# Kernel tuning notes

Hardware: AMD Instinct MI355X
Metric: run time of the kernel (lower is better)

## Reference

```python
import jax, jax.numpy as jnp
import numpy as np

N_NODES = 25000
N_EDGES = 400000
CHANNELS = 32
EDGE_FEAT_DIM = 8
HIDDEN = 64
NUM_IRREPS = 4  # messages irreps = 2x0e + 2x1o -> 4 irreps, dim 8
AVG_NUM_NEIGHBORS = 16.0


def _mlp(x, W0, W1, W2, W3):
    # e3nn MultiLayerPerceptron: dense layers with 1/sqrt(fan_in) forward
    # normalization, silu on hidden layers, no output activation.
    for W in (W0, W1, W2):
        x = jax.nn.silu(x @ (W / jnp.sqrt(jnp.float32(W.shape[0]))))
    return x @ (W3 / jnp.sqrt(jnp.float32(W3.shape[0])))


def setup_inputs() -> dict:
    key = jax.random.key(0)
    ks = jax.random.split(key, 9)
    node_feats = jax.random.normal(ks[0], (N_NODES, CHANNELS, 4), jnp.float32)
    edge_attrs = jax.random.normal(ks[1], (N_EDGES, 4), jnp.float32)
    edge_feats = jax.random.normal(ks[2], (N_EDGES, EDGE_FEAT_DIM), jnp.float32)
    senders = jax.random.randint(ks[3], (N_EDGES,), 0, N_NODES)
    receivers = jax.random.randint(ks[4], (N_EDGES,), 0, N_NODES)
    W0 = jax.random.normal(ks[5], (EDGE_FEAT_DIM, HIDDEN), jnp.float32)
    W1 = jax.random.normal(ks[6], (HIDDEN, HIDDEN), jnp.float32)
    W2 = jax.random.normal(ks[7], (HIDDEN, HIDDEN), jnp.float32)
    W3 = jax.random.normal(ks[8], (HIDDEN, CHANNELS * NUM_IRREPS), jnp.float32)
    return {"node_feats": node_feats, "edge_attrs": edge_attrs,
            "edge_feats": edge_feats, "senders": senders, "receivers": receivers,
            "W0": W0, "W1": W1, "W2": W2, "W3": W3}


def reference(node_feats, edge_attrs, edge_feats, senders, receivers, W0, W1, W2, W3):
    # Gather sender node features: [E, C, 4] with irreps 0e (dim1) + 1o (dim3)
    x = node_feats[senders]
    s, v = x[..., 0], x[..., 1:4]            # [E,C], [E,C,3]
    a_s = edge_attrs[:, 0]                   # Y_0: [E]
    a_v = edge_attrs[:, 1:4]                 # Y_1: [E,3]

    # CG tensor product filtered to 0e + 1o (e3nn normalization: sqrt(2l3+1)*w3j)
    m0a = s * a_s[:, None]                                   # 0e x 0e -> 0e  [E,C]
    m0b = jnp.einsum('ecd,ed->ec', v, a_v) / jnp.sqrt(3.0)   # 1o x 1o -> 0e  [E,C]
    m1a = s[..., None] * a_v[:, None, :]                     # 0e x 1o -> 1o  [E,C,3]
    m1b = v * a_s[:, None, None]                             # 1o x 0e -> 1o  [E,C,3]

    # Edge MLP gate: [E, C*num_irreps] -> mul_to_axis -> [E, C, num_irreps]
    mix = _mlp(edge_feats, W0, W1, W2, W3).reshape(N_EDGES, CHANNELS, NUM_IRREPS)

    # Elementwise tensor product with 4x0e scalars: per-irrep gating
    out_s = jnp.stack([m0a * mix[..., 0], m0b * mix[..., 1]], axis=-1)          # [E,C,2]
    out_v = jnp.concatenate([m1a * mix[..., 2:3], m1b * mix[..., 3:4]], axis=-1)  # [E,C,6]
    messages = jnp.concatenate([out_s, out_v], axis=-1)                          # [E,C,8]

    # Scatter-add into receivers, then normalize by sqrt(avg_num_neighbors)
    agg = jax.ops.segment_sum(messages, receivers, num_segments=N_NODES)
    return agg / jnp.sqrt(AVG_NUM_NEIGHBORS)
```

## Files before the change

kernel.cpp:

```cpp
#include <hip/hip_runtime.h>
#include <hip/hip_fp16.h>

#define NE 400000
#define NN 25000
#define MAXDEG 56
#define LDS_STRIDE 65

typedef __attribute__((ext_vector_type(8))) _Float16 half8;
typedef __attribute__((ext_vector_type(4))) _Float16 half4;
typedef __attribute__((ext_vector_type(4))) float f32x4;

#define WS_MIX_OFF   0ull
#define WS_SLOTS_OFF 102400000ull
#define WS_CNT_OFF   108000000ull
#define WS_WBUF_OFF  108100000ull
#define WS_NEED      108136864ull

#define WB_L0 0
#define WB_L1 2048
#define WB_L2 6144
#define WB_L3 10240

__device__ __forceinline__ float fast_silu(float x) {
    float e = __expf(-x);
    return x * __builtin_amdgcn_rcpf(1.0f + e);
}

__global__ __launch_bounds__(64) void prep_weights(
    const float* __restrict__ W0, const float* __restrict__ W1,
    const float* __restrict__ W2, const float* __restrict__ W3,
    _Float16* __restrict__ wbuf)
{
    const int f    = blockIdx.x;
    const int lane = threadIdx.x;
    const int n    = lane & 15;
    const int quad = lane >> 4;

    const float* W; int K, N, kt, nt, fl, base; float scale;
    if (f < 4)       { W = W0; K = 8;  N = 64;  fl = f;      kt = 0;       nt = fl;     scale = 0.35355339059327373f; base = WB_L0; }
    else if (f < 12) { W = W1; K = 64; N = 64;  fl = f - 4;  kt = fl >> 2; nt = fl & 3; scale = 0.125f;   base = WB_L1; }
    else if (f < 20) { W = W2; K = 64; N = 64;  fl = f - 12; kt = fl >> 2; nt = fl & 3; scale = 0.125f;   base = WB_L2; }
    else             { W = W3; K = 64; N = 128; fl = f - 20; kt = fl >> 3; nt = fl & 7; scale = 0.03125f; base = WB_L3; }

    _Float16 v[8];
    #pragma unroll
    for (int j = 0; j < 8; ++j) {
        const int k = kt * 32 + quad * 8 + j;
        const float val = (k < K) ? W[k * N + nt * 16 + n] * scale : 0.0f;
        v[j] = (_Float16)val;
    }
    *(half8*)(wbuf + base + fl * 512 + lane * 8) = *(const half8*)v;
}

__global__ __launch_bounds__(256) void build_kernel(
    const int* __restrict__ receivers, int* __restrict__ cnt, int* __restrict__ slots)
{
    int e = blockIdx.x * 256 + threadIdx.x;
    if (e >= NE) return;
    int r = receivers[e];
    int s = atomicAdd(&cnt[r], 1);
    if (s < MAXDEG) slots[r * MAXDEG + s] = e;
}

#define HS 72
__global__ __launch_bounds__(256) void mlp_mfma_kernel(
    const float*    __restrict__ edge_feats,
    const _Float16* __restrict__ wbuf,
    _Float16*       __restrict__ mix16)
{
    __shared__ _Float16 H[4 * 16 * HS];
    const int wave = threadIdx.x >> 6;
    const int lane = threadIdx.x & 63;
    const int col  = lane & 15;
    const int quad = lane >> 4;
    const int e0   = (blockIdx.x * 4 + wave) * 16;

    _Float16* Hw = &H[wave * 16 * HS];
    const half8* wb = (const half8*)wbuf;
    const f32x4 zero4 = {0.f, 0.f, 0.f, 0.f};

    half8 b0 = {0, 0, 0, 0, 0, 0, 0, 0};
    if (quad == 0) {
        const float4* efp = (const float4*)(edge_feats + (size_t)(e0 + col) * 8);
        const float4 x = efp[0], y = efp[1];
        b0[0] = (_Float16)x.x; b0[1] = (_Float16)x.y; b0[2] = (_Float16)x.z; b0[3] = (_Float16)x.w;
        b0[4] = (_Float16)y.x; b0[5] = (_Float16)y.y; b0[6] = (_Float16)y.z; b0[7] = (_Float16)y.w;
    }

    {
        #pragma unroll
        for (int nt = 0; nt < 4; ++nt) {
            f32x4 acc = __builtin_amdgcn_mfma_f32_16x16x32_f16(wb[(WB_L0 / 512 + nt) * 64 + lane], b0, zero4, 0, 0, 0);
            half4 h;
            #pragma unroll
            for (int r = 0; r < 4; ++r) h[r] = (_Float16)fast_silu(acc[r]);
            *(half4*)&Hw[col * HS + nt * 16 + quad * 4] = h;
        }
    }

    #pragma unroll
    for (int layer = 0; layer < 2; ++layer) {
        const int wbase = (layer == 0 ? WB_L1 : WB_L2) / 512;
        const half8 blo = *(const half8*)&Hw[col * HS + 0  + quad * 8];
        const half8 bhi = *(const half8*)&Hw[col * HS + 32 + quad * 8];
        f32x4 acc[4];
        #pragma unroll
        for (int nt = 0; nt < 4; ++nt) {
            acc[nt] = __builtin_amdgcn_mfma_f32_16x16x32_f16(wb[(wbase + 0 + nt) * 64 + lane], blo, zero4, 0, 0, 0);
            acc[nt] = __builtin_amdgcn_mfma_f32_16x16x32_f16(wb[(wbase + 4 + nt) * 64 + lane], bhi, acc[nt], 0, 0, 0);
        }
        #pragma unroll
        for (int nt = 0; nt < 4; ++nt) {
            half4 h;
            #pragma unroll
            for (int r = 0; r < 4; ++r) h[r] = (_Float16)fast_silu(acc[nt][r]);
            *(half4*)&Hw[col * HS + nt * 16 + quad * 4] = h;
        }
    }

    {
        const half8 blo = *(const half8*)&Hw[col * HS + 0  + quad * 8];
        const half8 bhi = *(const half8*)&Hw[col * HS + 32 + quad * 8];
        _Float16* mrow = mix16 + (size_t)(e0 + col) * 128;
        #pragma unroll
        for (int nt = 0; nt < 8; ++nt) {
            f32x4 acc = __builtin_amdgcn_mfma_f32_16x16x32_f16(wb[(WB_L3 / 512 + 0 + nt) * 64 + lane], blo, zero4, 0, 0, 0);
            acc = __builtin_amdgcn_mfma_f32_16x16x32_f16(wb[(WB_L3 / 512 + 8 + nt) * 64 + lane], bhi, acc, 0, 0, 0);
            half4 h;
            #pragma unroll
            for (int r = 0; r < 4; ++r) h[r] = (_Float16)acc[r];
            *(half4*)&mrow[nt * 16 + quad * 4] = h;
        }
    }
}

__global__ __launch_bounds__(64) void gather_kernel(
    const float*    __restrict__ node_feats,
    const float*    __restrict__ edge_attrs,
    const int*      __restrict__ senders,
    const _Float16* __restrict__ mix16,
    const int*      __restrict__ cnt,
    const int*      __restrict__ slots,
    float*          __restrict__ out)
{
    const int n    = blockIdx.x;
    const int lane = threadIdx.x;
    const int g    = lane >> 4;
    const int s    = lane & 15;
    const int c0   = 2 * s;
    const float inv_sqrt3 = 0.5773502691896258f;

    int d = cnt[n];
    if (d > MAXDEG) d = MAXDEG;
    const int* sl = slots + n * MAXDEG;

    float acc[16];
    #pragma unroll
    for (int j = 0; j < 16; ++j) acc[j] = 0.0f;

    #pragma unroll 2
    for (int base = 0; base < d; base += 4) {
        const int  ei  = base + g;
        const bool act = (ei < d);
        const int  eic = act ? ei : 0;
        const int  eid = sl[eic];
        const int  snd = senders[eid];
        const float4 a4v = ((const float4*)edge_attrs)[eid];
        const half8 m8 = *(const half8*)(mix16 + (size_t)eid * 128 + c0 * 4);
        const float4 xA = ((const float4*)(node_feats + (size_t)snd * 128))[c0];
        const float4 xB = ((const float4*)(node_feats + (size_t)snd * 128))[c0 + 1];

        const float z = act ? 1.0f : 0.0f;
        const float as = a4v.x, av0 = a4v.y, av1 = a4v.z, av2 = a4v.w;

        {
            const float m0 = z * (float)m8[0], m1 = z * (float)m8[1];
            const float m2 = z * (float)m8[2], m3 = z * (float)m8[3];
            const float sc = xA.x, v0 = xA.y, v1 = xA.z, v2 = xA.w;
            acc[0] = fmaf(sc * as, m0, acc[0]);
            const float dv = v0 * av0 + v1 * av1 + v2 * av2;
            acc[1] = fmaf(dv * inv_sqrt3, m1, acc[1]);
            acc[2] = fmaf(sc * av0, m2, acc[2]);
            acc[3] = fmaf(sc * av1, m2, acc[3]);
            acc[4] = fmaf(sc * av2, m2, acc[4]);
            acc[5] = fmaf(v0 * as, m3, acc[5]);
            acc[6] = fmaf(v1 * as, m3, acc[6]);
            acc[7] = fmaf(v2 * as, m3, acc[7]);
        }
        {
            const float m0 = z * (float)m8[4], m1 = z * (float)m8[5];
            const float m2 = z * (float)m8[6], m3 = z * (float)m8[7];
            const float sc = xB.x, v0 = xB.y, v1 = xB.z, v2 = xB.w;
            acc[8]  = fmaf(sc * as, m0, acc[8]);
            const float dv = v0 * av0 + v1 * av1 + v2 * av2;
            acc[9]  = fmaf(dv * inv_sqrt3, m1, acc[9]);
            acc[10] = fmaf(sc * av0, m2, acc[10]);
            acc[11] = fmaf(sc * av1, m2, acc[11]);
            acc[12] = fmaf(sc * av2, m2, acc[12]);
            acc[13] = fmaf(v0 * as, m3, acc[13]);
            acc[14] = fmaf(v1 * as, m3, acc[14]);
            acc[15] = fmaf(v2 * as, m3, acc[15]);
        }
    }

    #pragma unroll
    for (int j = 0; j < 16; ++j) {
        acc[j] += __shfl_xor(acc[j], 16, 64);
        acc[j] += __shfl_xor(acc[j], 32, 64);
    }

    if (g == 0) {
        float4* op = (float4*)(out + (size_t)n * 256 + s * 16);
        float4 r0; r0.x = acc[0];  r0.y = acc[1];  r0.z = acc[2];  r0.w = acc[3];
        float4 r1; r1.x = acc[4];  r1.y = acc[5];  r1.z = acc[6];  r1.w = acc[7];
        float4 r2; r2.x = acc[8];  r2.y = acc[9];  r2.z = acc[10]; r2.w = acc[11];
        float4 r3; r3.x = acc[12]; r3.y = acc[13]; r3.z = acc[14]; r3.w = acc[15];
        op[0] = r0; op[1] = r1; op[2] = r2; op[3] = r3;
    }
}

__global__ __launch_bounds__(128) void edge_mp_kernel(
    const float* __restrict__ node_feats, const float* __restrict__ edge_attrs,
    const float* __restrict__ edge_feats, const int* __restrict__ senders,
    const int* __restrict__ receivers, const float* __restrict__ W0,
    const float* __restrict__ W1, const float* __restrict__ W2,
    const float* __restrict__ W3, float* __restrict__ out)
{
    __shared__ float hbuf[128 * LDS_STRIDE];
    const int tid = threadIdx.x;
    const int e   = blockIdx.x * 128 + tid;
    if (e >= NE) return;
    float* hl = &hbuf[tid * LDS_STRIDE];

    float4 ef0 = ((const float4*)edge_feats)[e * 2 + 0];
    float4 ef1 = ((const float4*)edge_feats)[e * 2 + 1];
    float ef[8] = {ef0.x, ef0.y, ef0.z, ef0.w, ef1.x, ef1.y, ef1.z, ef1.w};
    float acc[64];
    #pragma unroll
    for (int i = 0; i < 64; ++i) acc[i] = 0.0f;
    #pragma unroll
    for (int j = 0; j < 8; ++j) {
        const float xj = ef[j];
        const float* wrow = W0 + j * 64;
        #pragma unroll
        for (int i = 0; i < 64; ++i) acc[i] = fmaf(xj, wrow[i], acc[i]);
    }
    {
        const float s0 = 0.35355339059327373f;
        #pragma unroll
        for (int i = 0; i < 64; ++i) hl[i] = fast_silu(acc[i] * s0);
    }
    #pragma unroll
    for (int i = 0; i < 64; ++i) acc[i] = 0.0f;
    #pragma unroll 4
    for (int j = 0; j < 64; ++j) {
        const float xj = hl[j];
        const float* wrow = W1 + j * 64;
        #pragma unroll
        for (int i = 0; i < 64; ++i) acc[i] = fmaf(xj, wrow[i], acc[i]);
    }
    #pragma unroll
    for (int i = 0; i < 64; ++i) hl[i] = fast_silu(acc[i] * 0.125f);
    #pragma unroll
    for (int i = 0; i < 64; ++i) acc[i] = 0.0f;
    #pragma unroll 4
    for (int j = 0; j < 64; ++j) {
        const float xj = hl[j];
        const float* wrow = W2 + j * 64;
        #pragma unroll
        for (int i = 0; i < 64; ++i) acc[i] = fmaf(xj, wrow[i], acc[i]);
    }
    float h2[64];
    #pragma unroll
    for (int i = 0; i < 64; ++i) h2[i] = fast_silu(acc[i] * 0.125f);

    const int snd = senders[e];
    const int rcv = receivers[e];
    const float4 a4 = ((const float4*)edge_attrs)[e];
    const float a_s = a4.x, av0 = a4.y, av1 = a4.z, av2 = a4.w;
    const float4* nf4 = (const float4*)(node_feats + (size_t)snd * 128);
    float* outp = out + (size_t)rcv * 256;
    const float mixscale = 0.03125f;
    const float inv_sqrt3 = 0.5773502691896258f;

    #pragma unroll 2
    for (int c = 0; c < 32; ++c) {
        float m0 = 0.0f, m1 = 0.0f, m2 = 0.0f, m3 = 0.0f;
        const float* wc = W3 + c * 4;
        #pragma unroll
        for (int j = 0; j < 64; ++j) {
            const float hj = h2[j];
            m0 = fmaf(hj, wc[j * 128 + 0], m0);
            m1 = fmaf(hj, wc[j * 128 + 1], m1);
            m2 = fmaf(hj, wc[j * 128 + 2], m2);
            m3 = fmaf(hj, wc[j * 128 + 3], m3);
        }
        m0 *= mixscale; m1 *= mixscale; m2 *= mixscale; m3 *= mixscale;
        const float4 x4 = nf4[c];
        const float s = x4.x, v0 = x4.y, v1 = x4.z, v2 = x4.w;
        float* op = outp + c * 8;
        atomicAdd(op + 0, s * a_s * m0);
        const float dotva = v0 * av0 + v1 * av1 + v2 * av2;
        atomicAdd(op + 1, dotva * inv_sqrt3 * m1);
        atomicAdd(op + 2, s * av0 * m2);
        atomicAdd(op + 3, s * av1 * m2);
        atomicAdd(op + 4, s * av2 * m2);
        atomicAdd(op + 5, v0 * a_s * m3);
        atomicAdd(op + 6, v1 * a_s * m3);
        atomicAdd(op + 7, v2 * a_s * m3);
    }
}

extern "C" void kernel_launch(void* const* d_in, const int* in_sizes, int n_in,
                              void* d_out, int out_size, void* d_ws, size_t ws_size,
                              hipStream_t stream) {
    const float* node_feats = (const float*)d_in[0];
    const float* edge_attrs = (const float*)d_in[1];
    const float* edge_feats = (const float*)d_in[2];
    const int*   senders    = (const int*)d_in[3];
    const int*   receivers  = (const int*)d_in[4];
    const float* W0 = (const float*)d_in[5];
    const float* W1 = (const float*)d_in[6];
    const float* W2 = (const float*)d_in[7];
    const float* W3 = (const float*)d_in[8];
    float* outp = (float*)d_out;

    if (ws_size >= WS_NEED) {
        char* w = (char*)d_ws;
        _Float16* mix16 = (_Float16*)(w + WS_MIX_OFF);
        int*      slots = (int*)(w + WS_SLOTS_OFF);
        int*      cnt   = (int*)(w + WS_CNT_OFF);
        _Float16* wbuf  = (_Float16*)(w + WS_WBUF_OFF);

        hipMemsetAsync(cnt, 0, NN * sizeof(int), stream);
        hipLaunchKernelGGL(prep_weights, dim3(36), dim3(64), 0, stream,
                           W0, W1, W2, W3, wbuf);
        hipLaunchKernelGGL(build_kernel, dim3((NE + 255) / 256), dim3(256), 0, stream,
                           receivers, cnt, slots);
        hipLaunchKernelGGL(mlp_mfma_kernel, dim3(NE / 64), dim3(256), 0, stream,
                           edge_feats, wbuf, mix16);
        hipLaunchKernelGGL(gather_kernel, dim3(NN), dim3(64), 0, stream,
                           node_feats, edge_attrs, senders, mix16, cnt, slots, outp);
    } else {
        hipMemsetAsync(d_out, 0, (size_t)out_size * sizeof(float), stream);
        hipLaunchKernelGGL(edge_mp_kernel, dim3((NE + 127) / 128), dim3(128), 0, stream,
                           node_feats, edge_attrs, edge_feats, senders, receivers,
                           W0, W1, W2, W3, outp);
    }
}
```

Before: 229.4 us.

## Fuse edge MLP into per-node gather kernel, dropping the mix buffer

Merges the edge MLP kernel into the receiver-sorted gather kernel. Each wave now handles one node, evaluates the MLP on MFMA for that node's incoming edges in tiles of 16, and stages the gates in LDS rather than writing and rereading a 100 MB fp16 mix array in global memory. The cost is that MFMA tiles are partly empty when a node's degree is not a multiple of 16, which adds extra MLP compute, and the per-node work becomes more serialized.

```diff
diff --git a/kernel.cpp b/kernel.cpp
--- a/kernel.cpp
+++ b/kernel.cpp
@@ -10,11 +10,10 @@
 typedef __attribute__((ext_vector_type(4))) _Float16 half4;
 typedef __attribute__((ext_vector_type(4))) float f32x4;
 
-#define WS_MIX_OFF   0ull
-#define WS_SLOTS_OFF 102400000ull
-#define WS_CNT_OFF   108000000ull
-#define WS_WBUF_OFF  108100000ull
-#define WS_NEED      108136864ull
+#define WS_SLOTS_OFF 0ull
+#define WS_CNT_OFF   5600000ull
+#define WS_WBUF_OFF  5700000ull
+#define WS_NEED      5736864ull
 
 #define WB_L0 0
 #define WB_L1 2048
@@ -63,143 +62,135 @@
 }
 
 #define HS 72
-__global__ __launch_bounds__(256) void mlp_mfma_kernel(
+#define MS 136
+__global__ __launch_bounds__(256) void fused_node_kernel(
+    const float*    __restrict__ node_feats,
+    const float*    __restrict__ edge_attrs,
     const float*    __restrict__ edge_feats,
+    const int*      __restrict__ senders,
     const _Float16* __restrict__ wbuf,
-    _Float16*       __restrict__ mix16)
+    const int*      __restrict__ cnt,
+    const int*      __restrict__ slots,
+    float*          __restrict__ out)
 {
     __shared__ _Float16 H[4 * 16 * HS];
+    __shared__ _Float16 Mx[4 * 16 * MS];
     const int wave = threadIdx.x >> 6;
     const int lane = threadIdx.x & 63;
     const int col  = lane & 15;
     const int quad = lane >> 4;
-    const int e0   = (blockIdx.x * 4 + wave) * 16;
+    const int n    = blockIdx.x * 4 + wave;
+    const float inv_sqrt3 = 0.5773502691896258f;
 
     _Float16* Hw = &H[wave * 16 * HS];
+    _Float16* Mw = &Mx[wave * 16 * MS];
     const half8* wb = (const half8*)wbuf;
     const f32x4 zero4 = {0.f, 0.f, 0.f, 0.f};
-
-    half8 b0 = {0, 0, 0, 0, 0, 0, 0, 0};
-    if (quad == 0) {
-        const float4* efp = (const float4*)(edge_feats + (size_t)(e0 + col) * 8);
-        const float4 x = efp[0], y = efp[1];
-        b0[0] = (_Float16)x.x; b0[1] = (_Float16)x.y; b0[2] = (_Float16)x.z; b0[3] = (_Float16)x.w;
-        b0[4] = (_Float16)y.x; b0[5] = (_Float16)y.y; b0[6] = (_Float16)y.z; b0[7] = (_Float16)y.w;
-    }
-
-    {
-        #pragma unroll
-        for (int nt = 0; nt < 4; ++nt) {
-            f32x4 acc = __builtin_amdgcn_mfma_f32_16x16x32_f16(wb[(WB_L0 / 512 + nt) * 64 + lane], b0, zero4, 0, 0, 0);
-            half4 h;
-            #pragma unroll
-            for (int r = 0; r < 4; ++r) h[r] = (_Float16)fast_silu(acc[r]);
-            *(half4*)&Hw[col * HS + nt * 16 + quad * 4] = h;
-        }
-    }
-
-    #pragma unroll
-    for (int layer = 0; layer < 2; ++layer) {
-        const int wbase = (layer == 0 ? WB_L1 : WB_L2) / 512;
-        const half8 blo = *(const half8*)&Hw[col * HS + 0  + quad * 8];
-        const half8 bhi = *(const half8*)&Hw[col * HS + 32 + quad * 8];
-        f32x4 acc[4];
-        #pragma unroll
-        for (int nt = 0; nt < 4; ++nt) {
-            acc[nt] = __builtin_amdgcn_mfma_f32_16x16x32_f16(wb[(wbase + 0 + nt) * 64 + lane], blo, zero4, 0, 0, 0);
-            acc[nt] = __builtin_amdgcn_mfma_f32_16x16x32_f16(wb[(wbase + 4 + nt) * 64 + lane], bhi, acc[nt], 0, 0, 0);
-        }
-        #pragma unroll
-        for (int nt = 0; nt < 4; ++nt) {
-            half4 h;
-            #pragma unroll
-            for (int r = 0; r < 4; ++r) h[r] = (_Float16)fast_silu(acc[nt][r]);
-            *(half4*)&Hw[col * HS + nt * 16 + quad * 4] = h;
-        }
-    }
-
-    {
-        const half8 blo = *(const half8*)&Hw[col * HS + 0  + quad * 8];
-        const half8 bhi = *(const half8*)&Hw[col * HS + 32 + quad * 8];
-        _Float16* mrow = mix16 + (size_t)(e0 + col) * 128;
-        #pragma unroll
-        for (int nt = 0; nt < 8; ++nt) {
-            f32x4 acc = __builtin_amdgcn_mfma_f32_16x16x32_f16(wb[(WB_L3 / 512 + 0 + nt) * 64 + lane], blo, zero4, 0, 0, 0);
-            acc = __builtin_amdgcn_mfma_f32_16x16x32_f16(wb[(WB_L3 / 512 + 8 + nt) * 64 + lane], bhi, acc, 0, 0, 0);
-            half4 h;
-            #pragma unroll
-            for (int r = 0; r < 4; ++r) h[r] = (_Float16)acc[r];
-            *(half4*)&mrow[nt * 16 + quad * 4] = h;
-        }
-    }
-}
-
-__global__ __launch_bounds__(64) void gather_kernel(
-    const float*    __restrict__ node_feats,
-    const float*    __restrict__ edge_attrs,
-    const int*      __restrict__ senders,
-    const _Float16* __restrict__ mix16,
-    const int*      __restrict__ cnt,
-    const int*      __restrict__ slots,
-    float*          __restrict__ out)
-{
-    const int n    = blockIdx.x;
-    const int lane = threadIdx.x;
-    const int g    = lane >> 4;
-    const int s    = lane & 15;
-    const int c0   = 2 * s;
-    const float inv_sqrt3 = 0.5773502691896258f;
 
     int d = cnt[n];
     if (d > MAXDEG) d = MAXDEG;
     const int* sl = slots + n * MAXDEG;
+    const int T = (d + 15) >> 4;
 
     float acc[16];
     #pragma unroll
     for (int j = 0; j < 16; ++j) acc[j] = 0.0f;
 
-    #pragma unroll 2
-    for (int base = 0; base < d; base += 4) {
-        const int  ei  = base + g;
-        const bool act = (ei < d);
-        const int  eic = act ? ei : 0;
-        const int  eid = sl[eic];
-        const int  snd = senders[eid];
-        const float4 a4v = ((const float4*)edge_attrs)[eid];
-        const half8 m8 = *(const half8*)(mix16 + (size_t)eid * 128 + c0 * 4);
-        const float4 xA = ((const float4*)(node_feats + (size_t)snd * 128))[c0];
-        const float4 xB = ((const float4*)(node_feats + (size_t)snd * 128))[c0 + 1];
-
-        const float z = act ? 1.0f : 0.0f;
-        const float as = a4v.x, av0 = a4v.y, av1 = a4v.z, av2 = a4v.w;
+    for (int t = 0; t < T; ++t) {
+        const int p0 = t * 16;
+
+        half8 b0 = {0, 0, 0, 0, 0, 0, 0, 0};
+        if (quad == 0 && p0 + col < d) {
+            const int e = sl[p0 + col];
+            const float4* efp = (const float4*)(edge_feats + (size_t)e * 8);
+            const float4 x = efp[0], y = efp[1];
+            b0[0] = (_Float16)x.x; b0[1] = (_Float16)x.y; b0[2] = (_Float16)x.z; b0[3] = (_Float16)x.w;
+            b0[4] = (_Float16)y.x; b0[5] = (_Float16)y.y; b0[6] = (_Float16)y.z; b0[7] = (_Float16)y.w;
+        }
+
+        #pragma unroll
+        for (int nt = 0; nt < 4; ++nt) {
+            f32x4 a = __builtin_amdgcn_mfma_f32_16x16x32_f16(wb[(WB_L0 / 512 + nt) * 64 + lane], b0, zero4, 0, 0, 0);
+            half4 h;
+            #pragma unroll
+            for (int r = 0; r < 4; ++r) h[r] = (_Float16)fast_silu(a[r]);
+            *(half4*)&Hw[col * HS + nt * 16 + quad * 4] = h;
+        }
+
+        #pragma unroll
+        for (int layer = 0; layer < 2; ++layer) {
+            const int wbase = (layer == 0 ? WB_L1 : WB_L2) / 512;
+            const half8 blo = *(const half8*)&Hw[col * HS + 0  + quad * 8];
+            const half8 bhi = *(const half8*)&Hw[col * HS + 32 + quad * 8];
+            f32x4 a4[4];
+            #pragma unroll
+            for (int nt = 0; nt < 4; ++nt) {
+                a4[nt] = __builtin_amdgcn_mfma_f32_16x16x32_f16(wb[(wbase + 0 + nt) * 64 + lane], blo, zero4, 0, 0, 0);
+                a4[nt] = __builtin_amdgcn_mfma_f32_16x16x32_f16(wb[(wbase + 4 + nt) * 64 + lane], bhi, a4[nt], 0, 0, 0);
+            }
+            #pragma unroll
+            for (int nt = 0; nt < 4; ++nt) {
+                half4 h;
+                #pragma unroll
+                for (int r = 0; r < 4; ++r) h[r] = (_Float16)fast_silu(a4[nt][r]);
+                *(half4*)&Hw[col * HS + nt * 16 + quad * 4] = h;
+            }
+        }
 
         {
-            const float m0 = z * (float)m8[0], m1 = z * (float)m8[1];
-            const float m2 = z * (float)m8[2], m3 = z * (float)m8[3];
-            const float sc = xA.x, v0 = xA.y, v1 = xA.z, v2 = xA.w;
-            acc[0] = fmaf(sc * as, m0, acc[0]);
-            const float dv = v0 * av0 + v1 * av1 + v2 * av2;
-            acc[1] = fmaf(dv * inv_sqrt3, m1, acc[1]);
-            acc[2] = fmaf(sc * av0, m2, acc[2]);
-            acc[3] = fmaf(sc * av1, m2, acc[3]);
-            acc[4] = fmaf(sc * av2, m2, acc[4]);
-            acc[5] = fmaf(v0 * as, m3, acc[5]);
-            acc[6] = fmaf(v1 * as, m3, acc[6]);
-            acc[7] = fmaf(v2 * as, m3, acc[7]);
-        }
-        {
-            const float m0 = z * (float)m8[4], m1 = z * (float)m8[5];
-            const float m2 = z * (float)m8[6], m3 = z * (float)m8[7];
-            const float sc = xB.x, v0 = xB.y, v1 = xB.z, v2 = xB.w;
-            acc[8]  = fmaf(sc * as, m0, acc[8]);
-            const float dv = v0 * av0 + v1 * av1 + v2 * av2;
-            acc[9]  = fmaf(dv * inv_sqrt3, m1, acc[9]);
-            acc[10] = fmaf(sc * av0, m2, acc[10]);
-            acc[11] = fmaf(sc * av1, m2, acc[11]);
-            acc[12] = fmaf(sc * av2, m2, acc[12]);
-            acc[13] = fmaf(v0 * as, m3, acc[13]);
-            acc[14] = fmaf(v1 * as, m3, acc[14]);
-            acc[15] = fmaf(v2 * as, m3, acc[15]);
+            const half8 blo = *(const half8*)&Hw[col * HS + 0  + quad * 8];
+            const half8 bhi = *(const half8*)&Hw[col * HS + 32 + quad * 8];
+            #pragma unroll
+            for (int nt = 0; nt < 8; ++nt) {
+                f32x4 a = __builtin_amdgcn_mfma_f32_16x16x32_f16(wb[(WB_L3 / 512 + 0 + nt) * 64 + lane], blo, zero4, 0, 0, 0);
+                a = __builtin_amdgcn_mfma_f32_16x16x32_f16(wb[(WB_L3 / 512 + 8 + nt) * 64 + lane], bhi, a, 0, 0, 0);
+                half4 h;
+                #pragma unroll
+                for (int r = 0; r < 4; ++r) h[r] = (_Float16)a[r];
+                *(half4*)&Mw[col * MS + nt * 16 + quad * 4] = h;
+            }
+        }
+
+        const int lim = (d - p0 < 16) ? (d - p0) : 16;
+        for (int base = 0; base < lim; base += 4) {
+            const int p  = p0 + base + quad;
+            const int pc = (p < d) ? p : 0;
+            const int eid = sl[pc];
+            const int snd = senders[eid];
+            const float4 a4v = ((const float4*)edge_attrs)[eid];
+            const half8 m8 = *(const half8*)&Mw[(base + quad) * MS + col * 8];
+            const float4 xA = ((const float4*)(node_feats + (size_t)snd * 128))[col * 2];
+            const float4 xB = ((const float4*)(node_feats + (size_t)snd * 128))[col * 2 + 1];
+            const float as = a4v.x, av0 = a4v.y, av1 = a4v.z, av2 = a4v.w;
+
+            {
+                const float m0 = (float)m8[0], m1 = (float)m8[1];
+                const float m2 = (float)m8[2], m3 = (float)m8[3];
+                const float sc = xA.x, v0 = xA.y, v1 = xA.z, v2 = xA.w;
+                acc[0] = fmaf(sc * as, m0, acc[0]);
+                const float dv = v0 * av0 + v1 * av1 + v2 * av2;
+                acc[1] = fmaf(dv * inv_sqrt3, m1, acc[1]);
+                acc[2] = fmaf(sc * av0, m2, acc[2]);
+                acc[3] = fmaf(sc * av1, m2, acc[3]);
+                acc[4] = fmaf(sc * av2, m2, acc[4]);
+                acc[5] = fmaf(v0 * as, m3, acc[5]);
+                acc[6] = fmaf(v1 * as, m3, acc[6]);
+                acc[7] = fmaf(v2 * as, m3, acc[7]);
+            }
+            {
+                const float m0 = (float)m8[4], m1 = (float)m8[5];
+                const float m2 = (float)m8[6], m3 = (float)m8[7];
+                const float sc = xB.x, v0 = xB.y, v1 = xB.z, v2 = xB.w;
+                acc[8]  = fmaf(sc * as, m0, acc[8]);
+                const float dv = v0 * av0 + v1 * av1 + v2 * av2;
+                acc[9]  = fmaf(dv * inv_sqrt3, m1, acc[9]);
+                acc[10] = fmaf(sc * av0, m2, acc[10]);
+                acc[11] = fmaf(sc * av1, m2, acc[11]);
+                acc[12] = fmaf(sc * av2, m2, acc[12]);
+                acc[13] = fmaf(v0 * as, m3, acc[13]);
+                acc[14] = fmaf(v1 * as, m3, acc[14]);
+                acc[15] = fmaf(v2 * as, m3, acc[15]);
+            }
         }
     }
 
@@ -209,8 +200,8 @@
         acc[j] += __shfl_xor(acc[j], 32, 64);
     }
 
-    if (g == 0) {
-        float4* op = (float4*)(out + (size_t)n * 256 + s * 16);
+    if (quad == 0) {
+        float4* op = (float4*)(out + (size_t)n * 256 + col * 16);
         float4 r0; r0.x = acc[0];  r0.y = acc[1];  r0.z = acc[2];  r0.w = acc[3];
         float4 r1; r1.x = acc[4];  r1.y = acc[5];  r1.z = acc[6];  r1.w = acc[7];
         float4 r2; r2.x = acc[8];  r2.y = acc[9];  r2.z = acc[10]; r2.w = acc[11];
@@ -327,7 +318,6 @@
 
     if (ws_size >= WS_NEED) {
         char* w = (char*)d_ws;
-        _Float16* mix16 = (_Float16*)(w + WS_MIX_OFF);
         int*      slots = (int*)(w + WS_SLOTS_OFF);
         int*      cnt   = (int*)(w + WS_CNT_OFF);
         _Float16* wbuf  = (_Float16*)(w + WS_WBUF_OFF);
@@ -337,10 +327,9 @@
                            W0, W1, W2, W3, wbuf);
         hipLaunchKernelGGL(build_kernel, dim3((NE + 255) / 256), dim3(256), 0, stream,
                            receivers, cnt, slots);
-        hipLaunchKernelGGL(mlp_mfma_kernel, dim3(NE / 64), dim3(256), 0, stream,
-                           edge_feats, wbuf, mix16);
-        hipLaunchKernelGGL(gather_kernel, dim3(NN), dim3(64), 0, stream,
-                           node_feats, edge_attrs, senders, mix16, cnt, slots, outp);
+        hipLaunchKernelGGL(fused_node_kernel, dim3(NN / 4), dim3(256), 0, stream,
+                           node_feats, edge_attrs, edge_feats, senders,
+                           wbuf, cnt, slots, outp);
     } else {
         hipMemsetAsync(d_out, 0, (size_t)out_size * sizeof(float), stream);
         hipLaunchKernelGGL(edge_mp_kernel, dim3((NE + 127) / 128), dim3(128), 0, stream,
```

Result: slower. 264.9 us (+15.5%).

## Fuse slot building into MLP kernel, fold count reset, double edge tile per wave

Applied to the files above, without the earlier changes.

The receiver-slot building (atomic count plus slot write) moves into the MLP kernel, and the count memset moves into the weight-prep kernel, removing two launches. Each wave now runs the MLP for 32 edges instead of 16, reusing each loaded weight fragment for two MFMA tiles and halving the grid. The trade-off is higher register and LDS use per block, which can lower occupancy, and atomics mixed into the MFMA kernel.

```diff
diff --git a/kernel.cpp b/kernel.cpp
--- a/kernel.cpp
+++ b/kernel.cpp
@@ -29,10 +29,13 @@
 __global__ __launch_bounds__(64) void prep_weights(
     const float* __restrict__ W0, const float* __restrict__ W1,
     const float* __restrict__ W2, const float* __restrict__ W3,
-    _Float16* __restrict__ wbuf)
+    _Float16* __restrict__ wbuf, int* __restrict__ cnt)
 {
     const int f    = blockIdx.x;
     const int lane = threadIdx.x;
+
+    for (int i = f * 64 + lane; i < NN; i += 36 * 64) cnt[i] = 0;
+
     const int n    = lane & 15;
     const int quad = lane >> 4;
 
@@ -52,84 +55,107 @@
     *(half8*)(wbuf + base + fl * 512 + lane * 8) = *(const half8*)v;
 }
 
-__global__ __launch_bounds__(256) void build_kernel(
-    const int* __restrict__ receivers, int* __restrict__ cnt, int* __restrict__ slots)
-{
-    int e = blockIdx.x * 256 + threadIdx.x;
-    if (e >= NE) return;
-    int r = receivers[e];
-    int s = atomicAdd(&cnt[r], 1);
-    if (s < MAXDEG) slots[r * MAXDEG + s] = e;
-}
-
 #define HS 72
-__global__ __launch_bounds__(256) void mlp_mfma_kernel(
+__global__ __launch_bounds__(256) void mlp_build_kernel(
     const float*    __restrict__ edge_feats,
+    const int*      __restrict__ receivers,
     const _Float16* __restrict__ wbuf,
+    int*            __restrict__ cnt,
+    int*            __restrict__ slots,
     _Float16*       __restrict__ mix16)
 {
-    __shared__ _Float16 H[4 * 16 * HS];
-    const int wave = threadIdx.x >> 6;
-    const int lane = threadIdx.x & 63;
+    __shared__ _Float16 H[4 * 2 * 16 * HS];
+    const int tid  = threadIdx.x;
+    const int wave = tid >> 6;
+    const int lane = tid & 63;
     const int col  = lane & 15;
     const int quad = lane >> 4;
-    const int e0   = (blockIdx.x * 4 + wave) * 16;
-
-    _Float16* Hw = &H[wave * 16 * HS];
+
+    if (tid < 128) {
+        const int e = blockIdx.x * 128 + tid;
+        const int r = receivers[e];
+        const int s = atomicAdd(&cnt[r], 1);
+        if (s < MAXDEG) slots[r * MAXDEG + s] = e;
+    }
+
+    const int e0 = (blockIdx.x * 4 + wave) * 32;
+    _Float16* HA = &H[wave * 2 * 16 * HS];
+    _Float16* HB = HA + 16 * HS;
     const half8* wb = (const half8*)wbuf;
     const f32x4 zero4 = {0.f, 0.f, 0.f, 0.f};
 
-    half8 b0 = {0, 0, 0, 0, 0, 0, 0, 0};
+    half8 b0A = {0, 0, 0, 0, 0, 0, 0, 0};
+    half8 b0B = {0, 0, 0, 0, 0, 0, 0, 0};
     if (quad == 0) {
-        const float4* efp = (const float4*)(edge_feats + (size_t)(e0 + col) * 8);
-        const float4 x = efp[0], y = efp[1];
-        b0[0] = (_Float16)x.x; b0[1] = (_Float16)x.y; b0[2] = (_Float16)x.z; b0[3] = (_Float16)x.w;
-        b0[4] = (_Float16)y.x; b0[5] = (_Float16)y.y; b0[6] = (_Float16)y.z; b0[7] = (_Float16)y.w;
-    }
-
-    {
-        #pragma unroll
-        for (int nt = 0; nt < 4; ++nt) {
-            f32x4 acc = __builtin_amdgcn_mfma_f32_16x16x32_f16(wb[(WB_L0 / 512 + nt) * 64 + lane], b0, zero4, 0, 0, 0);
-            half4 h;
-            #pragma unroll
-            for (int r = 0; r < 4; ++r) h[r] = (_Float16)fast_silu(acc[r]);
-            *(half4*)&Hw[col * HS + nt * 16 + quad * 4] = h;
-        }
+        const float4* pA = (const float4*)(edge_feats + (size_t)(e0 + col) * 8);
+        const float4 xa = pA[0], ya = pA[1];
+        b0A[0] = (_Float16)xa.x; b0A[1] = (_Float16)xa.y; b0A[2] = (_Float16)xa.z; b0A[3] = (_Float16)xa.w;
+        b0A[4] = (_Float16)ya.x; b0A[5] = (_Float16)ya.y; b0A[6] = (_Float16)ya.z; b0A[7] = (_Float16)ya.w;
+        const float4* pB = (const float4*)(edge_feats + (size_t)(e0 + 16 + col) * 8);
+        const float4 xb = pB[0], yb = pB[1];
+        b0B[0] = (_Float16)xb.x; b0B[1] = (_Float16)xb.y; b0B[2] = (_Float16)xb.z; b0B[3] = (_Float16)xb.w;
+        b0B[4] = (_Float16)yb.x; b0B[5] = (_Float16)yb.y; b0B[6] = (_Float16)yb.z; b0B[7] = (_Float16)yb.w;
+    }
+
+    #pragma unroll
+    for (int nt = 0; nt < 4; ++nt) {
+        const half8 w = wb[(WB_L0 / 512 + nt) * 64 + lane];
+        f32x4 aA = __builtin_amdgcn_mfma_f32_16x16x32_f16(w, b0A, zero4, 0, 0, 0);
+        f32x4 aB = __builtin_amdgcn_mfma_f32_16x16x32_f16(w, b0B, zero4, 0, 0, 0);
+        half4 hA, hB;
+        #pragma unroll
+        for (int r = 0; r < 4; ++r) { hA[r] = (_Float16)fast_silu(aA[r]); hB[r] = (_Float16)fast_silu(aB[r]); }
+        *(half4*)&HA[col * HS + nt * 16 + quad * 4] = hA;
+        *(half4*)&HB[col * HS + nt * 16 + quad * 4] = hB;
     }
 
     #pragma unroll
     for (int layer = 0; layer < 2; ++layer) {
         const int wbase = (layer == 0 ? WB_L1 : WB_L2) / 512;
-        const half8 blo = *(const half8*)&Hw[col * HS + 0  + quad * 8];
-        const half8 bhi = *(const half8*)&Hw[col * HS + 32 + quad * 8];
-        f32x4 acc[4];
+        const half8 bloA = *(const half8*)&HA[col * HS + 0  + quad * 8];
+        const half8 bhiA = *(const half8*)&HA[col * HS + 32 + quad * 8];
+        const half8 bloB = *(const half8*)&HB[col * HS + 0  + quad * 8];
+        const half8 bhiB = *(const half8*)&HB[col * HS + 32 + quad * 8];
+        f32x4 aA[4], aB[4];
         #pragma unroll
         for (int nt = 0; nt < 4; ++nt) {
-            acc[nt] = __builtin_amdgcn_mfma_f32_16x16x32_f16(wb[(wbase + 0 + nt) * 64 + lane], blo, zero4, 0, 0, 0);
-            acc[nt] = __builtin_amdgcn_mfma_f32_16x16x32_f16(wb[(wbase + 4 + nt) * 64 + lane], bhi, acc[nt], 0, 0, 0);
+            const half8 wlo = wb[(wbase + 0 + nt) * 64 + lane];
+            const half8 whi = wb[(wbase + 4 + nt) * 64 + lane];
+            aA[nt] = __builtin_amdgcn_mfma_f32_16x16x32_f16(wlo, bloA, zero4, 0, 0, 0);
+            aA[nt] = __builtin_amdgcn_mfma_f32_16x16x32_f16(whi, bhiA, aA[nt], 0, 0, 0);
+            aB[nt] = __builtin_amdgcn_mfma_f32_16x16x32_f16(wlo, bloB, zero4, 0, 0, 0);
+            aB[nt] = __builtin_amdgcn_mfma_f32_16x16x32_f16(whi, bhiB, aB[nt], 0, 0, 0);
         }
         #pragma unroll
         for (int nt = 0; nt < 4; ++nt) {
-            half4 h;
+            half4 hA, hB;
             #pragma unroll
-            for (int r = 0; r < 4; ++r) h[r] = (_Float16)fast_silu(acc[nt][r]);
-            *(half4*)&Hw[col * HS + nt * 16 + quad * 4] = h;
+            for (int r = 0; r < 4; ++r) { hA[r] = (_Float16)fast_silu(aA[nt][r]); hB[r] = (_Float16)fast_silu(aB[nt][r]); }
+            *(half4*)&HA[col * HS + nt * 16 + quad * 4] = hA;
+            *(half4*)&HB[col * HS + nt * 16 + quad * 4] = hB;
         }
     }
 
     {
-        const half8 blo = *(const half8*)&Hw[col * HS + 0  + quad * 8];
-        const half8 bhi = *(const half8*)&Hw[col * HS + 32 + quad * 8];
-        _Float16* mrow = mix16 + (size_t)(e0 + col) * 128;
+        const half8 bloA = *(const half8*)&HA[col * HS + 0  + quad * 8];
+        const half8 bhiA = *(const half8*)&HA[col * HS + 32 + quad * 8];
+        const half8 bloB = *(const half8*)&HB[col * HS + 0  + quad * 8];
+        const half8 bhiB = *(const half8*)&HB[col * HS + 32 + quad * 8];
+        _Float16* mrowA = mix16 + (size_t)(e0 + col) * 128;
+        _Float16* mrowB = mix16 + (size_t)(e0 + 16 + col) * 128;
         #pragma unroll
         for (int nt = 0; nt < 8; ++nt) {
-            f32x4 acc = __builtin_amdgcn_mfma_f32_16x16x32_f16(wb[(WB_L3 / 512 + 0 + nt) * 64 + lane], blo, zero4, 0, 0, 0);
-            acc = __builtin_amdgcn_mfma_f32_16x16x32_f16(wb[(WB_L3 / 512 + 8 + nt) * 64 + lane], bhi, acc, 0, 0, 0);
-            half4 h;
+            const half8 wlo = wb[(WB_L3 / 512 + 0 + nt) * 64 + lane];
+            const half8 whi = wb[(WB_L3 / 512 + 8 + nt) * 64 + lane];
+            f32x4 aA = __builtin_amdgcn_mfma_f32_16x16x32_f16(wlo, bloA, zero4, 0, 0, 0);
+            aA = __builtin_amdgcn_mfma_f32_16x16x32_f16(whi, bhiA, aA, 0, 0, 0);
+            f32x4 aB = __builtin_amdgcn_mfma_f32_16x16x32_f16(wlo, bloB, zero4, 0, 0, 0);
+            aB = __builtin_amdgcn_mfma_f32_16x16x32_f16(whi, bhiB, aB, 0, 0, 0);
+            half4 hA, hB;
             #pragma unroll
-            for (int r = 0; r < 4; ++r) h[r] = (_Float16)acc[r];
-            *(half4*)&mrow[nt * 16 + quad * 4] = h;
+            for (int r = 0; r < 4; ++r) { hA[r] = (_Float16)aA[r]; hB[r] = (_Float16)aB[r]; }
+            *(half4*)&mrowA[nt * 16 + quad * 4] = hA;
+            *(half4*)&mrowB[nt * 16 + quad * 4] = hB;
         }
     }
 }
@@ -332,13 +358,10 @@
         int*      cnt   = (int*)(w + WS_CNT_OFF);
         _Float16* wbuf  = (_Float16*)(w + WS_WBUF_OFF);
 
-        hipMemsetAsync(cnt, 0, NN * sizeof(int), stream);
         hipLaunchKernelGGL(prep_weights, dim3(36), dim3(64), 0, stream,
-                           W0, W1, W2, W3, wbuf);
-        hipLaunchKernelGGL(build_kernel, dim3((NE + 255) / 256), dim3(256), 0, stream,
-                           receivers, cnt, slots);
-        hipLaunchKernelGGL(mlp_mfma_kernel, dim3(NE / 64), dim3(256), 0, stream,
-                           edge_feats, wbuf, mix16);
+                           W0, W1, W2, W3, wbuf, cnt);
+        hipLaunchKernelGGL(mlp_build_kernel, dim3(NE / 128), dim3(256), 0, stream,
+                           edge_feats, receivers, wbuf, cnt, slots, mix16);
         hipLaunchKernelGGL(gather_kernel, dim3(NN), dim3(64), 0, stream,
                            node_feats, edge_attrs, senders, mix16, cnt, slots, outp);
     } else {
```

New measurement: 211.0 us. 1.09x faster.

## Fuse receiver bucketing into MLP kernel and widen gather to eight edges

Applied to the files above, without the earlier changes.

Zeroing the per-node counters moves into the weight-prep kernel, and the receiver bucketing with atomics moves into the MLP kernel. That removes a memset and a separate kernel launch. The gather kernel is reorganised so each 64-lane block handles eight edges per iteration, with each lane covering four channels instead of two. This halves the loop trip count for average-degree nodes and issues wider loads. In exchange each lane holds more accumulator registers and needs an extra cross-lane shuffle step, and it drops the explicit unroll.

```diff
diff --git a/kernel.cpp b/kernel.cpp
--- a/kernel.cpp
+++ b/kernel.cpp
@@ -29,10 +29,13 @@
 __global__ __launch_bounds__(64) void prep_weights(
     const float* __restrict__ W0, const float* __restrict__ W1,
     const float* __restrict__ W2, const float* __restrict__ W3,
-    _Float16* __restrict__ wbuf)
+    _Float16* __restrict__ wbuf, int* __restrict__ cnt)
 {
     const int f    = blockIdx.x;
     const int lane = threadIdx.x;
+
+    for (int i = f * 64 + lane; i < NN; i += 36 * 64) cnt[i] = 0;
+
     const int n    = lane & 15;
     const int quad = lane >> 4;
 
@@ -52,29 +55,32 @@
     *(half8*)(wbuf + base + fl * 512 + lane * 8) = *(const half8*)v;
 }
 
-__global__ __launch_bounds__(256) void build_kernel(
-    const int* __restrict__ receivers, int* __restrict__ cnt, int* __restrict__ slots)
-{
-    int e = blockIdx.x * 256 + threadIdx.x;
-    if (e >= NE) return;
-    int r = receivers[e];
-    int s = atomicAdd(&cnt[r], 1);
-    if (s < MAXDEG) slots[r * MAXDEG + s] = e;
-}
-
 #define HS 72
-__global__ __launch_bounds__(256) void mlp_mfma_kernel(
+__global__ __launch_bounds__(256) void mlp_build_kernel(
     const float*    __restrict__ edge_feats,
+    const int*      __restrict__ receivers,
     const _Float16* __restrict__ wbuf,
+    int*            __restrict__ cnt,
+    int*            __restrict__ slots,
     _Float16*       __restrict__ mix16)
 {
     __shared__ _Float16 H[4 * 16 * HS];
-    const int wave = threadIdx.x >> 6;
-    const int lane = threadIdx.x & 63;
+    const int tid  = threadIdx.x;
+    const int wave = tid >> 6;
+    const int lane = tid & 63;
     const int col  = lane & 15;
     const int quad = lane >> 4;
-    const int e0   = (blockIdx.x * 4 + wave) * 16;
-
+
+    {
+        const int e = blockIdx.x * 256 + tid;
+        if (e < NE) {
+            const int r = receivers[e];
+            const int s = atomicAdd(&cnt[r], 1);
+            if (s < MAXDEG) slots[r * MAXDEG + s] = e;
+        }
+    }
+
+    const int e0 = (blockIdx.x * 4 + wave) * 16;
     _Float16* Hw = &H[wave * 16 * HS];
     const half8* wb = (const half8*)wbuf;
     const f32x4 zero4 = {0.f, 0.f, 0.f, 0.f};
@@ -145,77 +151,69 @@
 {
     const int n    = blockIdx.x;
     const int lane = threadIdx.x;
-    const int g    = lane >> 4;
-    const int s    = lane & 15;
-    const int c0   = 2 * s;
+    const int g    = lane >> 3;
+    const int s    = lane & 7;
+    const int c0   = 4 * s;
     const float inv_sqrt3 = 0.5773502691896258f;
 
     int d = cnt[n];
     if (d > MAXDEG) d = MAXDEG;
     const int* sl = slots + n * MAXDEG;
 
-    float acc[16];
-    #pragma unroll
-    for (int j = 0; j < 16; ++j) acc[j] = 0.0f;
-
-    #pragma unroll 2
-    for (int base = 0; base < d; base += 4) {
+    float acc[32];
+    #pragma unroll
+    for (int j = 0; j < 32; ++j) acc[j] = 0.0f;
+
+    for (int base = 0; base < d; base += 8) {
         const int  ei  = base + g;
         const bool act = (ei < d);
         const int  eic = act ? ei : 0;
         const int  eid = sl[eic];
         const int  snd = senders[eid];
         const float4 a4v = ((const float4*)edge_attrs)[eid];
-        const half8 m8 = *(const half8*)(mix16 + (size_t)eid * 128 + c0 * 4);
-        const float4 xA = ((const float4*)(node_feats + (size_t)snd * 128))[c0];
-        const float4 xB = ((const float4*)(node_feats + (size_t)snd * 128))[c0 + 1];
-
+        const half8* mp = (const half8*)(mix16 + (size_t)eid * 128 + c0 * 4);
+        const half8 mA = mp[0];
+        const half8 mB = mp[1];
+        const float4* nf = (const float4*)(node_feats + (size_t)snd * 128);
         const float z = act ? 1.0f : 0.0f;
         const float as = a4v.x, av0 = a4v.y, av1 = a4v.z, av2 = a4v.w;
 
-        {
-            const float m0 = z * (float)m8[0], m1 = z * (float)m8[1];
-            const float m2 = z * (float)m8[2], m3 = z * (float)m8[3];
-            const float sc = xA.x, v0 = xA.y, v1 = xA.z, v2 = xA.w;
-            acc[0] = fmaf(sc * as, m0, acc[0]);
+        #pragma unroll
+        for (int k = 0; k < 4; ++k) {
+            const float m0 = z * (float)((k & 1) ? ((k < 2) ? mA[4] : mB[4]) : ((k < 2) ? mA[0] : mB[0]));
+            const float m1 = z * (float)((k & 1) ? ((k < 2) ? mA[5] : mB[5]) : ((k < 2) ? mA[1] : mB[1]));
+            const float m2 = z * (float)((k & 1) ? ((k < 2) ? mA[6] : mB[6]) : ((k < 2) ? mA[2] : mB[2]));
+            const float m3 = z * (float)((k & 1) ? ((k < 2) ? mA[7] : mB[7]) : ((k < 2) ? mA[3] : mB[3]));
+            const float4 x4 = nf[c0 + k];
+            const float sc = x4.x, v0 = x4.y, v1 = x4.z, v2 = x4.w;
+            float* a = &acc[k * 8];
+            a[0] = fmaf(sc * as, m0, a[0]);
             const float dv = v0 * av0 + v1 * av1 + v2 * av2;
-            acc[1] = fmaf(dv * inv_sqrt3, m1, acc[1]);
-            acc[2] = fmaf(sc * av0, m2, acc[2]);
-            acc[3] = fmaf(sc * av1, m2, acc[3]);
-            acc[4] = fmaf(sc * av2, m2, acc[4]);
-            acc[5] = fmaf(v0 * as, m3, acc[5]);
-            acc[6] = fmaf(v1 * as, m3, acc[6]);
-            acc[7] = fmaf(v2 * as, m3, acc[7]);
-        }
-        {
-            const float m0 = z * (float)m8[4], m1 = z * (float)m8[5];
-            const float m2 = z * (float)m8[6], m3 = z * (float)m8[7];
-            const float sc = xB.x, v0 = xB.y, v1 = xB.z, v2 = xB.w;
-            acc[8]  = fmaf(sc * as, m0, acc[8]);
-            const float dv = v0 * av0 + v1 * av1 + v2 * av2;
-            acc[9]  = fmaf(dv * inv_sqrt3, m1, acc[9]);
-            acc[10] = fmaf(sc * av0, m2, acc[10]);
-            acc[11] = fmaf(sc * av1, m2, acc[11]);
-            acc[12] = fmaf(sc * av2, m2, acc[12]);
-            acc[13] = fmaf(v0 * as, m3, acc[13]);
-            acc[14] = fmaf(v1 * as, m3, acc[14]);
-            acc[15] = fmaf(v2 * as, m3, acc[15]);
-        }
-    }
-
-    #pragma unroll
-    for (int j = 0; j < 16; ++j) {
+            a[1] = fmaf(dv * inv_sqrt3, m1, a[1]);
+            a[2] = fmaf(sc * av0, m2, a[2]);
+            a[3] = fmaf(sc * av1, m2, a[3]);
+            a[4] = fmaf(sc * av2, m2, a[4]);
+            a[5] = fmaf(v0 * as, m3, a[5]);
+            a[6] = fmaf(v1 * as, m3, a[6]);
+            a[7] = fmaf(v2 * as, m3, a[7]);
+        }
+    }
+
+    #pragma unroll
+    for (int j = 0; j < 32; ++j) {
+        acc[j] += __shfl_xor(acc[j], 8, 64);
         acc[j] += __shfl_xor(acc[j], 16, 64);
         acc[j] += __shfl_xor(acc[j], 32, 64);
     }
 
     if (g == 0) {
-        float4* op = (float4*)(out + (size_t)n * 256 + s * 16);
-        float4 r0; r0.x = acc[0];  r0.y = acc[1];  r0.z = acc[2];  r0.w = acc[3];
-        float4 r1; r1.x = acc[4];  r1.y = acc[5];  r1.z = acc[6];  r1.w = acc[7];
-        float4 r2; r2.x = acc[8];  r2.y = acc[9];  r2.z = acc[10]; r2.w = acc[11];
-        float4 r3; r3.x = acc[12]; r3.y = acc[13]; r3.z = acc[14]; r3.w = acc[15];
-        op[0] = r0; op[1] = r1; op[2] = r2; op[3] = r3;
+        float4* op = (float4*)(out + (size_t)n * 256 + s * 32);
+        #pragma unroll
+        for (int q = 0; q < 8; ++q) {
+            float4 r; r.x = acc[q * 4 + 0]; r.y = acc[q * 4 + 1];
+            r.z = acc[q * 4 + 2]; r.w = acc[q * 4 + 3];
+            op[q] = r;
+        }
     }
 }
 
@@ -332,13 +330,10 @@
         int*      cnt   = (int*)(w + WS_CNT_OFF);
         _Float16* wbuf  = (_Float16*)(w + WS_WBUF_OFF);
 
-        hipMemsetAsync(cnt, 0, NN * sizeof(int), stream);
         hipLaunchKernelGGL(prep_weights, dim3(36), dim3(64), 0, stream,
-                           W0, W1, W2, W3, wbuf);
-        hipLaunchKernelGGL(build_kernel, dim3((NE + 255) / 256), dim3(256), 0, stream,
-                           receivers, cnt, slots);
-        hipLaunchKernelGGL(mlp_mfma_kernel, dim3(NE / 64), dim3(256), 0, stream,
-                           edge_feats, wbuf, mix16);
+                           W0, W1, W2, W3, wbuf, cnt);
+        hipLaunchKernelGGL(mlp_build_kernel, dim3(NE / 64), dim3(256), 0, stream,
+                           edge_feats, receivers, wbuf, cnt, slots, mix16);
         hipLaunchKernelGGL(gather_kernel, dim3(NN), dim3(64), 0, stream,
                            node_feats, edge_attrs, senders, mix16, cnt, slots, outp);
     } else {
```

After: 223.8 us. 2.4% less time.
